# Kernel tuning notes

Hardware: AMD Instinct MI355X
Metric: run time of the kernel (lower is better)

The kernel has to match this reference:

```python
import jax, jax.numpy as jnp
import numpy as np

E = 3_200_000
D = 16
N = 100_000


def setup_inputs() -> dict:
    key = jax.random.key(0)
    k1, k2 = jax.random.split(key)
    x = jax.random.normal(k1, (E, D), dtype=jnp.float32)
    edge_dst = jax.random.randint(k2, (E,), 0, N, dtype=jnp.int64)
    return {"x": x, "edge_dst": edge_dst, "num_nodes": N}


def reference(x, edge_dst, num_nodes):
    # sum_over_neighbours: scatter-add edge features to destination atoms -> [N, D]
    summed = jax.ops.segment_sum(x, edge_dst, num_segments=num_nodes)
    # number_of_neighbours(include_central_atom=True): per-atom edge count + 1
    counts = jax.ops.segment_sum(
        jnp.ones((x.shape[0],), dtype=x.dtype), edge_dst, num_segments=num_nodes
    ) + jnp.asarray(1.0, dtype=x.dtype)
    # left_aligned_div by sqrt(counts): broadcast counts over trailing feature dims
    return summed / jnp.sqrt(counts)[:, None]
```

## Files before the change

kernel.cpp:

```cpp
#include <hip/hip_runtime.h>

#define DFEAT 16
#define NPB 64
#define NPB_SHIFT 6
#define EB 16384
#define BIN_THREADS 512
#define BATCH (EB / BIN_THREADS)
#define SORT_CAP 3072

__global__ void na_bin_kernel(const int* __restrict__ edge_dst,
                              int* __restrict__ hist,
                              int E, int B, int nblocks) {
    extern __shared__ int h[];
    const int b = blockIdx.x;
    const int t = threadIdx.x;
    for (int i = t; i < B; i += BIN_THREADS) h[i] = 0;
    __syncthreads();
    const int base = b * EB;

    #pragma unroll
    for (int c = 0; c < BATCH; c += 8) {
        int d[8];
        #pragma unroll
        for (int jj = 0; jj < 8; ++jj) {
            int e = base + (c + jj) * BIN_THREADS + t;
            d[jj] = (e < E) ? edge_dst[e] : -1;
        }
        #pragma unroll
        for (int jj = 0; jj < 8; ++jj)
            if (d[jj] >= 0) atomicAdd(&h[d[jj] >> NPB_SHIFT], 1);
    }
    __syncthreads();
    for (int i = t; i < B; i += BIN_THREADS)
        hist[(size_t)i * nblocks + b] = h[i];
}

__global__ void na_row_scan(int* __restrict__ hist,
                            int* __restrict__ bucketTotal,
                            int nblocks) {
    const int k = blockIdx.x;
    const int t = threadIdx.x;
    int* row = hist + (size_t)k * nblocks;
    const int CPT = (nblocks + 63) >> 6;
    const int beg = min(t * CPT, nblocks);
    const int end = min(beg + CPT, nblocks);

    int s = 0;
    for (int i = beg; i < end; ++i) s += row[i];
    int inc = s;
    #pragma unroll
    for (int d = 1; d < 64; d <<= 1) {
        int u = __shfl_up(inc, d);
        if (t >= d) inc += u;
    }
    int run = inc - s;
    for (int i = beg; i < end; ++i) {
        int c = row[i];
        row[i] = run;
        run += c;
    }
    if (t == 63) bucketTotal[k] = inc;
}

__global__ void na_base_scan(const int* __restrict__ bucketTotal,
                             int* __restrict__ bucketBase,
                             int B) {
    __shared__ int lds[1024];
    const int t = threadIdx.x;
    const int CPT = (B + 1023) >> 10;
    const int beg = min(t * CPT, B);
    const int end = min(beg + CPT, B);
    int s = 0;
    for (int i = beg; i < end; ++i) s += bucketTotal[i];
    lds[t] = s;
    __syncthreads();
    for (int off = 1; off < 1024; off <<= 1) {
        int add = (t >= off) ? lds[t - off] : 0;
        __syncthreads();
        lds[t] += add;
        __syncthreads();
    }
    int run = lds[t] - s;
    for (int i = beg; i < end; ++i) {
        int c = bucketTotal[i];
        bucketBase[i] = run;
        run += c;
    }
    if (t == 1023) bucketBase[B] = lds[1023];
}

__global__ void na_scatter_fused(const int* __restrict__ edge_dst,
                                 const int* __restrict__ hist,
                                 const int* __restrict__ bucketBase,
                                 int* __restrict__ binned,
                                 int E, int B, int nblocks) {
    extern __shared__ int h[];
    const int b = blockIdx.x;
    const int t = threadIdx.x;
    for (int i = t; i < B; i += BIN_THREADS)
        h[i] = bucketBase[i] + hist[(size_t)i * nblocks + b];
    __syncthreads();
    const int base = b * EB;

    #pragma unroll
    for (int c = 0; c < BATCH; c += 8) {
        int d[8];
        #pragma unroll
        for (int jj = 0; jj < 8; ++jj) {
            int e = base + (c + jj) * BIN_THREADS + t;
            d[jj] = (e < E) ? edge_dst[e] : -1;
        }
        #pragma unroll
        for (int jj = 0; jj < 8; ++jj) {
            if (d[jj] >= 0) {
                int n = d[jj];
                int e = base + (c + jj) * BIN_THREADS + t;
                int pos = atomicAdd(&h[n >> NPB_SHIFT], 1);
                binned[pos] = ((n & (NPB - 1)) << 22) | e;
            }
        }
    }
}

__global__ __launch_bounds__(256, 7)
void na_sort_gather(const float* __restrict__ x,
                    const int* __restrict__ binned,
                    const int* __restrict__ bucketBase,
                    float* __restrict__ out,
                    int N) {
    __shared__ int sorted[SORT_CAP];
    __shared__ int cnt[NPB];
    __shared__ int cur[NPB];
    __shared__ int excl[NPB + 1];

    const int k = blockIdx.x;
    const int t = threadIdx.x;

    const int beg = bucketBase[k];
    const int end = bucketBase[k + 1];
    const int sz = end - beg;

    if (t < NPB) { cnt[t] = 0; cur[t] = 0; }
    __syncthreads();

    if (sz <= SORT_CAP) {
        for (int j = t; j < sz; j += 256)
            atomicAdd(&cnt[binned[beg + j] >> 22], 1);
        __syncthreads();
        if (t < 64) {
            int v = cnt[t];
            int inc = v;
            #pragma unroll
            for (int d = 1; d < 64; d <<= 1) {
                int u = __shfl_up(inc, d);
                if (t >= d) inc += u;
            }
            excl[t] = inc - v;
            if (t == 63) excl[NPB] = inc;
        }
        __syncthreads();
        for (int j = t; j < sz; j += 256) {
            int v = binned[beg + j];
            int d = v >> 22;
            int r = atomicAdd(&cur[d], 1);
            sorted[excl[d] + r] = v & 0x3FFFFF;
        }
        __syncthreads();

        const int g = t >> 4;
        const int lane16 = t & 15;
        const int es = lane16 >> 2;
        const int q = lane16 & 3;
        const float4* x4 = reinterpret_cast<const float4*>(x);

        for (int ln = g; ln < NPB; ln += 16) {
            int n = k * NPB + ln;
            if (n >= N) break;
            int lbeg = excl[ln], lend = excl[ln + 1];
            float ax = 0.f, ay = 0.f, az = 0.f, aw = 0.f;

            int i = lbeg + es;
            for (; i + 12 < lend; i += 16) {
                int e0 = sorted[i];
                int e1 = sorted[i + 4];
                int e2 = sorted[i + 8];
                int e3 = sorted[i + 12];
                float4 v0 = x4[(size_t)e0 * 4 + q];
                float4 v1 = x4[(size_t)e1 * 4 + q];
                float4 v2 = x4[(size_t)e2 * 4 + q];
                float4 v3 = x4[(size_t)e3 * 4 + q];
                ax += (v0.x + v1.x) + (v2.x + v3.x);
                ay += (v0.y + v1.y) + (v2.y + v3.y);
                az += (v0.z + v1.z) + (v2.z + v3.z);
                aw += (v0.w + v1.w) + (v2.w + v3.w);
            }
            for (; i < lend; i += 4) {
                int e0 = sorted[i];
                float4 v0 = x4[(size_t)e0 * 4 + q];
                ax += v0.x; ay += v0.y; az += v0.z; aw += v0.w;
            }

            ax += __shfl_xor(ax, 4); ay += __shfl_xor(ay, 4);
            az += __shfl_xor(az, 4); aw += __shfl_xor(aw, 4);
            ax += __shfl_xor(ax, 8); ay += __shfl_xor(ay, 8);
            az += __shfl_xor(az, 8); aw += __shfl_xor(aw, 8);

            float s = rsqrtf((float)(lend - lbeg) + 1.0f);
            if (es == 0) {
                float4 r; r.x = ax * s; r.y = ay * s; r.z = az * s; r.w = aw * s;
                reinterpret_cast<float4*>(out)[(size_t)n * 4 + q] = r;
            }
        }
    } else {
        const int ln = t >> 2;
        const int q = t & 3;
        const float4* x4 = reinterpret_cast<const float4*>(x);
        int n = k * NPB + ln;
        if (n < N) {
            float ax = 0.f, ay = 0.f, az = 0.f, aw = 0.f;
            int deg = 0;
            for (int j = 0; j < sz; ++j) {
                int v = binned[beg + j];
                if ((v >> 22) == ln) {
                    float4 vv = x4[(size_t)(v & 0x3FFFFF) * 4 + q];
                    ax += vv.x; ay += vv.y; az += vv.z; aw += vv.w;
                    ++deg;
                }
            }
            float s = rsqrtf((float)deg + 1.0f);
            float4 r; r.x = ax * s; r.y = ay * s; r.z = az * s; r.w = aw * s;
            reinterpret_cast<float4*>(out)[(size_t)n * 4 + q] = r;
        }
    }
}

extern "C" void kernel_launch(void* const* d_in, const int* in_sizes, int n_in,
                              void* d_out, int out_size, void* d_ws, size_t ws_size,
                              hipStream_t stream) {
    const float* x        = (const float*)d_in[0];
    const int*   edge_dst = (const int*)d_in[1];
    float*       out      = (float*)d_out;

    const int E = in_sizes[1];
    const int N = out_size / DFEAT;
    const int B = (N + NPB - 1) >> NPB_SHIFT;
    const int nblocks = (E + EB - 1) / EB;
    const int M = B * nblocks;

    int* binned      = (int*)d_ws;
    int* hist        = binned + E;
    int* bucketTotal = hist + M;
    int* bucketBase  = bucketTotal + B;

    na_bin_kernel<<<nblocks, BIN_THREADS, B * sizeof(int), stream>>>(
        edge_dst, hist, E, B, nblocks);
    na_row_scan<<<B, 64, 0, stream>>>(hist, bucketTotal, nblocks);
    na_base_scan<<<1, 1024, 0, stream>>>(bucketTotal, bucketBase, B);
    na_scatter_fused<<<nblocks, BIN_THREADS, B * sizeof(int), stream>>>(
        edge_dst, hist, bucketBase, binned, E, B, nblocks);
    na_sort_gather<<<B, 256, 0, stream>>>(x, binned, bucketBase, out, N);
}
```

Measured before the change: 120.4 us.

## Shrink bin blocks, transpose histogram layout, stage bucket entries in registers, unroll gather deeper

Halves the edges and threads per binning block, so there are more, smaller blocks. The histogram becomes block-major, which makes the writes from the bin and scatter kernels coalesced but leaves the row scan reading with a stride. The sort-gather kernel now loads each bucket's binned entries into registers once and reuses them for both the count and placement passes instead of reading them from global memory twice. The gather loop is unrolled to eight independent loads per thread for more memory-level parallelism, at the cost of more registers.

Measured after the change: 130.5 us. +8.4%, slower.

```diff
diff --git a/kernel.cpp b/kernel.cpp
--- a/kernel.cpp
+++ b/kernel.cpp
@@ -3,14 +3,15 @@
 #define DFEAT 16
 #define NPB 64
 #define NPB_SHIFT 6
-#define EB 16384
-#define BIN_THREADS 512
+#define EB 8192
+#define BIN_THREADS 256
 #define BATCH (EB / BIN_THREADS)
 #define SORT_CAP 3072
+#define VSTAGE (SORT_CAP / 256)
 
 __global__ void na_bin_kernel(const int* __restrict__ edge_dst,
                               int* __restrict__ hist,
-                              int E, int B, int nblocks) {
+                              int E, int B) {
     extern __shared__ int h[];
     const int b = blockIdx.x;
     const int t = threadIdx.x;
@@ -32,21 +33,20 @@
     }
     __syncthreads();
     for (int i = t; i < B; i += BIN_THREADS)
-        hist[(size_t)i * nblocks + b] = h[i];
+        hist[(size_t)b * B + i] = h[i];
 }
 
 __global__ void na_row_scan(int* __restrict__ hist,
                             int* __restrict__ bucketTotal,
-                            int nblocks) {
+                            int B, int nblocks) {
     const int k = blockIdx.x;
     const int t = threadIdx.x;
-    int* row = hist + (size_t)k * nblocks;
     const int CPT = (nblocks + 63) >> 6;
     const int beg = min(t * CPT, nblocks);
     const int end = min(beg + CPT, nblocks);
 
     int s = 0;
-    for (int i = beg; i < end; ++i) s += row[i];
+    for (int j = beg; j < end; ++j) s += hist[(size_t)j * B + k];
     int inc = s;
     #pragma unroll
     for (int d = 1; d < 64; d <<= 1) {
@@ -54,9 +54,9 @@
         if (t >= d) inc += u;
     }
     int run = inc - s;
-    for (int i = beg; i < end; ++i) {
-        int c = row[i];
-        row[i] = run;
+    for (int j = beg; j < end; ++j) {
+        int c = hist[(size_t)j * B + k];
+        hist[(size_t)j * B + k] = run;
         run += c;
     }
     if (t == 63) bucketTotal[k] = inc;
@@ -93,12 +93,12 @@
                                  const int* __restrict__ hist,
                                  const int* __restrict__ bucketBase,
                                  int* __restrict__ binned,
-                                 int E, int B, int nblocks) {
+                                 int E, int B) {
     extern __shared__ int h[];
     const int b = blockIdx.x;
     const int t = threadIdx.x;
     for (int i = t; i < B; i += BIN_THREADS)
-        h[i] = bucketBase[i] + hist[(size_t)i * nblocks + b];
+        h[i] = bucketBase[i] + hist[(size_t)b * B + i];
     __syncthreads();
     const int base = b * EB;
 
@@ -144,26 +144,35 @@
     __syncthreads();
 
     if (sz <= SORT_CAP) {
-        for (int j = t; j < sz; j += 256)
-            atomicAdd(&cnt[binned[beg + j] >> 22], 1);
+        int v[VSTAGE];
+        #pragma unroll
+        for (int c = 0; c < VSTAGE; ++c) {
+            int j = c * 256 + t;
+            v[c] = (j < sz) ? binned[beg + j] : -1;
+        }
+        #pragma unroll
+        for (int c = 0; c < VSTAGE; ++c)
+            if (v[c] >= 0) atomicAdd(&cnt[v[c] >> 22], 1);
         __syncthreads();
         if (t < 64) {
-            int v = cnt[t];
-            int inc = v;
+            int cv = cnt[t];
+            int inc = cv;
             #pragma unroll
             for (int d = 1; d < 64; d <<= 1) {
                 int u = __shfl_up(inc, d);
                 if (t >= d) inc += u;
             }
-            excl[t] = inc - v;
+            excl[t] = inc - cv;
             if (t == 63) excl[NPB] = inc;
         }
         __syncthreads();
-        for (int j = t; j < sz; j += 256) {
-            int v = binned[beg + j];
-            int d = v >> 22;
-            int r = atomicAdd(&cur[d], 1);
-            sorted[excl[d] + r] = v & 0x3FFFFF;
+        #pragma unroll
+        for (int c = 0; c < VSTAGE; ++c) {
+            if (v[c] >= 0) {
+                int d = v[c] >> 22;
+                int r = atomicAdd(&cur[d], 1);
+                sorted[excl[d] + r] = v[c] & 0x3FFFFF;
+            }
         }
         __syncthreads();
 
@@ -180,19 +189,27 @@
             float ax = 0.f, ay = 0.f, az = 0.f, aw = 0.f;
 
             int i = lbeg + es;
-            for (; i + 12 < lend; i += 16) {
+            for (; i + 28 < lend; i += 32) {
                 int e0 = sorted[i];
                 int e1 = sorted[i + 4];
                 int e2 = sorted[i + 8];
                 int e3 = sorted[i + 12];
+                int e4 = sorted[i + 16];
+                int e5 = sorted[i + 20];
+                int e6 = sorted[i + 24];
+                int e7 = sorted[i + 28];
                 float4 v0 = x4[(size_t)e0 * 4 + q];
                 float4 v1 = x4[(size_t)e1 * 4 + q];
                 float4 v2 = x4[(size_t)e2 * 4 + q];
                 float4 v3 = x4[(size_t)e3 * 4 + q];
-                ax += (v0.x + v1.x) + (v2.x + v3.x);
-                ay += (v0.y + v1.y) + (v2.y + v3.y);
-                az += (v0.z + v1.z) + (v2.z + v3.z);
-                aw += (v0.w + v1.w) + (v2.w + v3.w);
+                float4 v4 = x4[(size_t)e4 * 4 + q];
+                float4 v5 = x4[(size_t)e5 * 4 + q];
+                float4 v6 = x4[(size_t)e6 * 4 + q];
+                float4 v7 = x4[(size_t)e7 * 4 + q];
+                ax += ((v0.x + v1.x) + (v2.x + v3.x)) + ((v4.x + v5.x) + (v6.x + v7.x));
+                ay += ((v0.y + v1.y) + (v2.y + v3.y)) + ((v4.y + v5.y) + (v6.y + v7.y));
+                az += ((v0.z + v1.z) + (v2.z + v3.z)) + ((v4.z + v5.z) + (v6.z + v7.z));
+                aw += ((v0.w + v1.w) + (v2.w + v3.w)) + ((v4.w + v5.w) + (v6.w + v7.w));
             }
             for (; i < lend; i += 4) {
                 int e0 = sorted[i];
@@ -220,10 +237,10 @@
             float ax = 0.f, ay = 0.f, az = 0.f, aw = 0.f;
             int deg = 0;
             for (int j = 0; j < sz; ++j) {
-                int v = binned[beg + j];
-                if ((v >> 22) == ln) {
-                    float4 vv = x4[(size_t)(v & 0x3FFFFF) * 4 + q];
-                    ax += vv.x; ay += vv.y; az += vv.z; aw += vv.w;
+                int vv = binned[beg + j];
+                if ((vv >> 22) == ln) {
+                    float4 xv = x4[(size_t)(vv & 0x3FFFFF) * 4 + q];
+                    ax += xv.x; ay += xv.y; az += xv.z; aw += xv.w;
                     ++deg;
                 }
             }
@@ -253,10 +270,10 @@
     int* bucketBase  = bucketTotal + B;
 
     na_bin_kernel<<<nblocks, BIN_THREADS, B * sizeof(int), stream>>>(
-        edge_dst, hist, E, B, nblocks);
-    na_row_scan<<<B, 64, 0, stream>>>(hist, bucketTotal, nblocks);
+        edge_dst, hist, E, B);
+    na_row_scan<<<B, 64, 0, stream>>>(hist, bucketTotal, B, nblocks);
     na_base_scan<<<1, 1024, 0, stream>>>(bucketTotal, bucketBase, B);
     na_scatter_fused<<<nblocks, BIN_THREADS, B * sizeof(int), stream>>>(
-        edge_dst, hist, bucketBase, binned, E, B, nblocks);
+        edge_dst, hist, bucketBase, binned, E, B);
     na_sort_gather<<<B, 256, 0, stream>>>(x, binned, bucketBase, out, N);
 }
```

## Use nontemporal vector loads, byte offsets, and a single-wave base scan

Applied to the files above, without the earlier changes.

The base scan is replaced by a single 64-lane wave doing a shuffle scan instead of a 1024-thread LDS scan with many barriers. In the gather, edge indices are stored pre-shifted as byte offsets, which removes the 64-bit multiply per load. The x loads and output stores now use nontemporal builtins on ext_vector float4. The offset shift (e<<6) fits in int only while E stays below 2^25, and nontemporal hints may cost cache locality for x rows that are reused.

Result: slower. 132.4 us (+10.0%).

```diff
diff --git a/kernel.cpp b/kernel.cpp
--- a/kernel.cpp
+++ b/kernel.cpp
@@ -8,6 +8,8 @@
 #define BATCH (EB / BIN_THREADS)
 #define SORT_CAP 3072
 
+typedef float f32x4 __attribute__((ext_vector_type(4)));
+
 __global__ void na_bin_kernel(const int* __restrict__ edge_dst,
                               int* __restrict__ hist,
                               int E, int B, int nblocks) {
@@ -65,28 +67,25 @@
 __global__ void na_base_scan(const int* __restrict__ bucketTotal,
                              int* __restrict__ bucketBase,
                              int B) {
-    __shared__ int lds[1024];
-    const int t = threadIdx.x;
-    const int CPT = (B + 1023) >> 10;
+    const int t = threadIdx.x;
+    const int CPT = (B + 63) >> 6;
     const int beg = min(t * CPT, B);
     const int end = min(beg + CPT, B);
     int s = 0;
     for (int i = beg; i < end; ++i) s += bucketTotal[i];
-    lds[t] = s;
-    __syncthreads();
-    for (int off = 1; off < 1024; off <<= 1) {
-        int add = (t >= off) ? lds[t - off] : 0;
-        __syncthreads();
-        lds[t] += add;
-        __syncthreads();
-    }
-    int run = lds[t] - s;
+    int inc = s;
+    #pragma unroll
+    for (int d = 1; d < 64; d <<= 1) {
+        int u = __shfl_up(inc, d);
+        if (t >= d) inc += u;
+    }
+    int run = inc - s;
     for (int i = beg; i < end; ++i) {
         int c = bucketTotal[i];
         bucketBase[i] = run;
         run += c;
     }
-    if (t == 1023) bucketBase[B] = lds[1023];
+    if (t == 63) bucketBase[B] = inc;
 }
 
 __global__ void na_scatter_fused(const int* __restrict__ edge_dst,
@@ -163,7 +162,7 @@
             int v = binned[beg + j];
             int d = v >> 22;
             int r = atomicAdd(&cur[d], 1);
-            sorted[excl[d] + r] = v & 0x3FFFFF;
+            sorted[excl[d] + r] = (v & 0x3FFFFF) << 6;
         }
         __syncthreads();
 
@@ -171,44 +170,42 @@
         const int lane16 = t & 15;
         const int es = lane16 >> 2;
         const int q = lane16 & 3;
-        const float4* x4 = reinterpret_cast<const float4*>(x);
+        const char* xb = reinterpret_cast<const char*>(x) + q * 16;
 
         for (int ln = g; ln < NPB; ln += 16) {
             int n = k * NPB + ln;
             if (n >= N) break;
             int lbeg = excl[ln], lend = excl[ln + 1];
-            float ax = 0.f, ay = 0.f, az = 0.f, aw = 0.f;
+            f32x4 acc = {0.f, 0.f, 0.f, 0.f};
 
             int i = lbeg + es;
             for (; i + 12 < lend; i += 16) {
-                int e0 = sorted[i];
-                int e1 = sorted[i + 4];
-                int e2 = sorted[i + 8];
-                int e3 = sorted[i + 12];
-                float4 v0 = x4[(size_t)e0 * 4 + q];
-                float4 v1 = x4[(size_t)e1 * 4 + q];
-                float4 v2 = x4[(size_t)e2 * 4 + q];
-                float4 v3 = x4[(size_t)e3 * 4 + q];
-                ax += (v0.x + v1.x) + (v2.x + v3.x);
-                ay += (v0.y + v1.y) + (v2.y + v3.y);
-                az += (v0.z + v1.z) + (v2.z + v3.z);
-                aw += (v0.w + v1.w) + (v2.w + v3.w);
+                int o0 = sorted[i];
+                int o1 = sorted[i + 4];
+                int o2 = sorted[i + 8];
+                int o3 = sorted[i + 12];
+                f32x4 v0 = __builtin_nontemporal_load((const f32x4*)(xb + o0));
+                f32x4 v1 = __builtin_nontemporal_load((const f32x4*)(xb + o1));
+                f32x4 v2 = __builtin_nontemporal_load((const f32x4*)(xb + o2));
+                f32x4 v3 = __builtin_nontemporal_load((const f32x4*)(xb + o3));
+                acc += (v0 + v1) + (v2 + v3);
             }
             for (; i < lend; i += 4) {
-                int e0 = sorted[i];
-                float4 v0 = x4[(size_t)e0 * 4 + q];
-                ax += v0.x; ay += v0.y; az += v0.z; aw += v0.w;
-            }
-
-            ax += __shfl_xor(ax, 4); ay += __shfl_xor(ay, 4);
-            az += __shfl_xor(az, 4); aw += __shfl_xor(aw, 4);
-            ax += __shfl_xor(ax, 8); ay += __shfl_xor(ay, 8);
-            az += __shfl_xor(az, 8); aw += __shfl_xor(aw, 8);
+                f32x4 v0 = __builtin_nontemporal_load((const f32x4*)(xb + sorted[i]));
+                acc += v0;
+            }
+
+            #pragma unroll
+            for (int c = 0; c < 4; ++c) {
+                acc[c] += __shfl_xor(acc[c], 4);
+                acc[c] += __shfl_xor(acc[c], 8);
+            }
 
             float s = rsqrtf((float)(lend - lbeg) + 1.0f);
             if (es == 0) {
-                float4 r; r.x = ax * s; r.y = ay * s; r.z = az * s; r.w = aw * s;
-                reinterpret_cast<float4*>(out)[(size_t)n * 4 + q] = r;
+                f32x4 r = acc * s;
+                __builtin_nontemporal_store(
+                    r, (f32x4*)(reinterpret_cast<char*>(out) + (size_t)n * 64 + q * 16));
             }
         }
     } else {
@@ -255,7 +252,7 @@
     na_bin_kernel<<<nblocks, BIN_THREADS, B * sizeof(int), stream>>>(
         edge_dst, hist, E, B, nblocks);
     na_row_scan<<<B, 64, 0, stream>>>(hist, bucketTotal, nblocks);
-    na_base_scan<<<1, 1024, 0, stream>>>(bucketTotal, bucketBase, B);
+    na_base_scan<<<1, 64, 0, stream>>>(bucketTotal, bucketBase, B);
     na_scatter_fused<<<nblocks, BIN_THREADS, B * sizeof(int), stream>>>(
         edge_dst, hist, bucketBase, binned, E, B, nblocks);
     na_sort_gather<<<B, 256, 0, stream>>>(x, binned, bucketBase, out, N);
```
